# Performance work log

Hardware: AMD Instinct MI355X
Metric: run time of the kernel (lower is better)

The kernel has to match this reference:

```python
import jax, jax.numpy as jnp
import numpy as np

BOX = 100.0      # points live in [0, BOX)^3
STRIDE = 128     # > BOX/voxel_size, used for linearizing 3D voxel coords


def setup_inputs() -> dict:
    key = jax.random.key(0)
    k1, k2 = jax.random.split(key)
    N, C = 2_000_000, 32
    positions = jax.random.uniform(k1, (N, 3), dtype=jnp.float32) * BOX
    features = jax.random.normal(k2, (N, C), dtype=jnp.float32)
    voxel_size = jnp.ones((), dtype=jnp.float32)
    return {"positions": positions, "features": features, "voxel_size": voxel_size}


def reference(positions, features, voxel_size):
    """VoxelPooling(position_fn='center', feature_fn='max').

    Output is padded to N rows (M <= N real voxels); `valid` marks real voxels.
    Voxel grid is aligned to the origin; pooled position is the voxel center.
    """
    N = positions.shape[0]
    # integer voxel coordinates (positions are non-negative here)
    coords = jnp.floor(positions / voxel_size).astype(jnp.int32)           # [N,3]
    lin = coords[:, 0] + STRIDE * coords[:, 1] + STRIDE * STRIDE * coords[:, 2]  # [N]
    # compact unique voxels; jit-compatible with fixed size=N, pad with -1
    uniq, inv = jnp.unique(lin, size=N, fill_value=-1, return_inverse=True)
    # per-voxel max over features (empty segments get dtype-min, masked below)
    pooled_features = jax.ops.segment_max(features, inv, num_segments=N)   # [N,C]
    # decode voxel coords from linear key -> voxel centers
    cz = uniq // (STRIDE * STRIDE)
    rem = uniq % (STRIDE * STRIDE)
    cy = rem // STRIDE
    cx = rem % STRIDE
    centers = (jnp.stack([cx, cy, cz], axis=-1).astype(positions.dtype) + 0.5) * voxel_size
    valid = uniq >= 0                                                      # [N]
    pooled_positions = jnp.where(valid[:, None], centers, 0.0)
    pooled_features = jnp.where(valid[:, None], pooled_features, 0.0)
    return pooled_positions, pooled_features, valid
```

## Files before the change

kernel.cpp:

```cpp
#include <hip/hip_runtime.h>
#include <stdint.h>

#define STRIDE 128
#define NVOX (STRIDE * STRIDE * STRIDE)
#define BINVOX 512
#define NBIN (NVOX / BINVOX)
#define HB 256
#define HT 1024

typedef unsigned long long u64;

__device__ __forceinline__ uint32_t enc_f32(float f) {
  uint32_t u = __float_as_uint(f);
  return (u & 0x80000000u) ? ~u : (u | 0x80000000u);
}
__device__ __forceinline__ float dec_f32(uint32_t e) {
  uint32_t u = (e & 0x80000000u) ? (e & 0x7fffffffu) : ~e;
  return __uint_as_float(u);
}

__global__ __launch_bounds__(HT) void k_hist(const float* __restrict__ pos,
                                             const float* __restrict__ vs_p,
                                             int* __restrict__ lin_arr,
                                             uint8_t* __restrict__ bytemap,
                                             uint32_t* __restrict__ hist, int n) {
  __shared__ uint32_t h[NBIN];
  int b = blockIdx.x, t = threadIdx.x;
  #pragma unroll
  for (int k = t; k < NBIN; k += HT) h[k] = 0u;
  __syncthreads();
  int chunk = (n + HB - 1) / HB;
  int i0 = b * chunk, i1 = min(n, i0 + chunk);
  float vs = vs_p[0];
  for (int i = i0 + t; i < i1; i += HT) {
    float x = pos[3 * (size_t)i + 0];
    float y = pos[3 * (size_t)i + 1];
    float z = pos[3 * (size_t)i + 2];
    int lin = (int)floorf(x / vs) + STRIDE * (int)floorf(y / vs) +
              STRIDE * STRIDE * (int)floorf(z / vs);
    lin_arr[i] = lin;
    bytemap[lin] = 1;
    atomicAdd(&h[lin >> 9], 1u);
  }
  __syncthreads();
  #pragma unroll
  for (int k = t; k < NBIN; k += HT) hist[(size_t)b * NBIN + k] = h[k];
}

__global__ void k_scanA(const uint32_t* __restrict__ hist,
                        const uint32_t* __restrict__ bytemap_w,
                        uint32_t* __restrict__ base2, u64* __restrict__ tot2) {
  int bin = blockIdx.x * blockDim.x + threadIdx.x;
  uint32_t run = 0;
  #pragma unroll 8
  for (int b = 0; b < HB; ++b) {
    base2[(size_t)b * NBIN + bin] = run;
    run += hist[(size_t)b * NBIN + bin];
  }
  const uint4* bp = (const uint4*)(bytemap_w) + (size_t)bin * 32;
  uint32_t occ = 0;
  #pragma unroll
  for (int k = 0; k < 32; ++k) {
    uint4 v = bp[k];
    occ += __popc(v.x) + __popc(v.y) + __popc(v.z) + __popc(v.w);
  }
  tot2[bin] = (u64)run | ((u64)occ << 32);
}

__global__ __launch_bounds__(1024) void k_scan64(const u64* __restrict__ in,
                                                 uint32_t* __restrict__ bin_base,
                                                 uint32_t* __restrict__ occ_base,
                                                 uint32_t* __restrict__ Mp) {
  __shared__ u64 s[1024];
  int t = threadIdx.x;
  u64 v[4], sum = 0;
  #pragma unroll
  for (int j = 0; j < 4; ++j) { v[j] = in[t * 4 + j]; sum += v[j]; }
  s[t] = sum;
  __syncthreads();
  for (int off = 1; off < 1024; off <<= 1) {
    u64 a = (t >= off) ? s[t - off] : 0ull;
    __syncthreads();
    s[t] += a;
    __syncthreads();
  }
  u64 run = s[t] - sum;
  #pragma unroll
  for (int j = 0; j < 4; ++j) {
    bin_base[t * 4 + j] = (uint32_t)run;
    occ_base[t * 4 + j] = (uint32_t)(run >> 32);
    run += v[j];
  }
  if (t == 1023) Mp[0] = (uint32_t)(s[1023] >> 32);
}

__global__ __launch_bounds__(HT) void k_part(const int* __restrict__ lin_arr,
                                             const uint32_t* __restrict__ bin_base,
                                             const uint32_t* __restrict__ base2,
                                             uint32_t* __restrict__ pairs, int n) {
  __shared__ uint32_t cur[NBIN];
  int b = blockIdx.x, t = threadIdx.x;
  #pragma unroll
  for (int k = t; k < NBIN; k += HT)
    cur[k] = bin_base[k] + base2[(size_t)b * NBIN + k];
  __syncthreads();
  int chunk = (n + HB - 1) / HB;
  int i0 = b * chunk, i1 = min(n, i0 + chunk);
  for (int i = i0 + t; i < i1; i += HT) {
    int lin = lin_arr[i];
    uint32_t slot = atomicAdd(&cur[lin >> 9], 1u);
    pairs[slot] = ((uint32_t)(lin & (BINVOX - 1)) << 21) | (uint32_t)i;
  }
}

__global__ __launch_bounds__(1024) void k_pool(
    const float* __restrict__ feat, const float* __restrict__ vs_p,
    const uint32_t* __restrict__ pairs, const uint32_t* __restrict__ bin_base,
    const u64* __restrict__ tot2, const uint32_t* __restrict__ occ_base,
    const uint8_t* __restrict__ bytemap,
    float* __restrict__ out_pos, float* __restrict__ out_feat,
    float* __restrict__ out_valid) {
  __shared__ uint32_t smax[BINVOX * 32];
  __shared__ u64 sbw[8];
  int bin = blockIdx.x;
  int t = threadIdx.x;
  uint32_t cnt = (uint32_t)tot2[bin];
  if (cnt == 0) return;
  uint32_t start = bin_base[bin];

  #pragma unroll
  for (int k = 0; k < 16; ++k) smax[t + k * 1024] = 0u;
  if (t < 512) {
    uint32_t occb = bytemap[(size_t)bin * BINVOX + t];
    u64 m = __ballot(occb != 0);
    if ((t & 63) == 0) sbw[t >> 6] = m;
  }
  __syncthreads();

  int g = t >> 5;
  int ch = t & 31;
  uint32_t last = cnt - 1;
  for (uint32_t u = (uint32_t)g; u < cnt; u += 256) {
    uint32_t p0 = pairs[start + u];
    uint32_t p1 = pairs[start + min(u + 32u, last)];
    uint32_t p2 = pairs[start + min(u + 64u, last)];
    uint32_t p3 = pairs[start + min(u + 96u, last)];
    uint32_t p4 = pairs[start + min(u + 128u, last)];
    uint32_t p5 = pairs[start + min(u + 160u, last)];
    uint32_t p6 = pairs[start + min(u + 192u, last)];
    uint32_t p7 = pairs[start + min(u + 224u, last)];
    float v0 = feat[(size_t)(p0 & 0x1FFFFFu) * 32 + ch];
    float v1 = feat[(size_t)(p1 & 0x1FFFFFu) * 32 + ch];
    float v2 = feat[(size_t)(p2 & 0x1FFFFFu) * 32 + ch];
    float v3 = feat[(size_t)(p3 & 0x1FFFFFu) * 32 + ch];
    float v4 = feat[(size_t)(p4 & 0x1FFFFFu) * 32 + ch];
    float v5 = feat[(size_t)(p5 & 0x1FFFFFu) * 32 + ch];
    float v6 = feat[(size_t)(p6 & 0x1FFFFFu) * 32 + ch];
    float v7 = feat[(size_t)(p7 & 0x1FFFFFu) * 32 + ch];
    atomicMax(&smax[(p0 >> 21) * 32 + ch], enc_f32(v0));
    atomicMax(&smax[(p1 >> 21) * 32 + ch], enc_f32(v1));
    atomicMax(&smax[(p2 >> 21) * 32 + ch], enc_f32(v2));
    atomicMax(&smax[(p3 >> 21) * 32 + ch], enc_f32(v3));
    atomicMax(&smax[(p4 >> 21) * 32 + ch], enc_f32(v4));
    atomicMax(&smax[(p5 >> 21) * 32 + ch], enc_f32(v5));
    atomicMax(&smax[(p6 >> 21) * 32 + ch], enc_f32(v6));
    atomicMax(&smax[(p7 >> 21) * 32 + ch], enc_f32(v7));
  }
  __syncthreads();

  int vb = t >> 1, half = t & 1;
  u64 w = sbw[vb >> 6];
  int bit = vb & 63;
  if ((w >> bit) & 1ull) {
    uint32_t lr = (uint32_t)__popcll(w & ((1ull << bit) - 1ull));
    for (int ww = 0; ww < (vb >> 6); ++ww) lr += (uint32_t)__popcll(sbw[ww]);
    uint32_t rank = occ_base[bin] + lr;
    float4* orow = (float4*)(out_feat + (size_t)rank * 32 + half * 16);
    #pragma unroll
    for (int j = 0; j < 4; ++j) {
      const uint32_t* sp = &smax[vb * 32 + half * 16 + j * 4];
      float4 o;
      o.x = dec_f32(sp[0]); o.y = dec_f32(sp[1]);
      o.z = dec_f32(sp[2]); o.w = dec_f32(sp[3]);
      orow[j] = o;
    }
    if (half == 0) {
      float vs = vs_p[0];
      int lin = bin * BINVOX + vb;
      int cx = lin & 127, cy = (lin >> 7) & 127, cz = lin >> 14;
      out_pos[(size_t)rank * 3 + 0] = ((float)cx + 0.5f) * vs;
      out_pos[(size_t)rank * 3 + 1] = ((float)cy + 0.5f) * vs;
      out_pos[(size_t)rank * 3 + 2] = ((float)cz + 0.5f) * vs;
      out_valid[rank] = 1.0f;
    }
  }
}

__global__ void k_tail(const uint32_t* __restrict__ Mp, float* __restrict__ out_pos,
                       float* __restrict__ out_feat, float* __restrict__ out_valid, int n) {
  size_t gid = (size_t)blockIdx.x * blockDim.x + threadIdx.x;
  int row = (int)(gid >> 3);
  int q = (int)(gid & 7);
  if (row >= n) return;
  uint32_t M = Mp[0];
  if ((uint32_t)row < M) return;
  ((float4*)out_feat)[(size_t)row * 8 + q] = make_float4(0.f, 0.f, 0.f, 0.f);
  if (q == 0) {
    out_pos[(size_t)row * 3 + 0] = 0.f;
    out_pos[(size_t)row * 3 + 1] = 0.f;
    out_pos[(size_t)row * 3 + 2] = 0.f;
    out_valid[row] = 0.f;
  }
}

extern "C" void kernel_launch(void* const* d_in, const int* in_sizes, int n_in,
                              void* d_out, int out_size, void* d_ws, size_t ws_size,
                              hipStream_t stream) {
  const float* pos  = (const float*)d_in[0];
  const float* feat = (const float*)d_in[1];
  const float* vs   = (const float*)d_in[2];
  int n = in_sizes[0] / 3;

  float*    out_pos   = (float*)d_out;
  uint32_t* out_feat  = (uint32_t*)(out_pos + (size_t)n * 3);
  float*    out_valid = (float*)((float*)out_feat + (size_t)n * 32);

  size_t scratch_u32 = 2 * (size_t)n + 2 * (size_t)HB * NBIN + 2 * (size_t)NBIN +
                       2 * (size_t)NBIN + NVOX / 4;
  uint32_t* scratch  = out_feat + (size_t)n * 32 - scratch_u32;
  int*      lin      = (int*)scratch;
  uint32_t* pairs    = scratch + n;
  uint32_t* hist     = pairs + n;
  uint32_t* base2    = hist + (size_t)HB * NBIN;
  u64*      tot2     = (u64*)(base2 + (size_t)HB * NBIN);
  uint32_t* bin_base = (uint32_t*)(tot2 + NBIN);
  uint32_t* occ_base = bin_base + NBIN;
  uint8_t*  bytemap  = (uint8_t*)(occ_base + NBIN);

  uint32_t* Mp = (uint32_t*)d_ws;

  hipMemsetAsync(bytemap, 0, (size_t)NVOX, stream);

  k_hist<<<HB, HT, 0, stream>>>(pos, vs, lin, bytemap, hist, n);
  k_scanA<<<NBIN / 256, 256, 0, stream>>>(hist, (const uint32_t*)bytemap, base2, tot2);
  k_scan64<<<1, 1024, 0, stream>>>(tot2, bin_base, occ_base, Mp);
  k_part<<<HB, HT, 0, stream>>>(lin, bin_base, base2, pairs, n);
  k_pool<<<NBIN, 1024, 0, stream>>>(feat, vs, pairs, bin_base, tot2, occ_base,
                                    bytemap, out_pos, (float*)out_feat, out_valid);
  k_tail<<<(int)(((size_t)n * 8 + 255) / 256), 256, 0, stream>>>(
      Mp, out_pos, (float*)out_feat, out_valid, n);
}
```

Baseline: 225.0 us.

## Fuse scan kernels with grid sync, fold tail into pool, drop bytemap memset

Merges the per-bin scan and the global scan into one multi-block kernel that exchanges segment totals through an atomic counter spin. The tail-zeroing work is appended as extra blocks of the pooling kernel. The bytemap memset is replaced by zeroing the scratch region at the end of each call, so the next call sees a cleared map. This cuts launches and a serial single-block scan, but relies on all scan blocks being co-resident and on the output buffer starting zeroed on the first call.

```diff
diff --git a/kernel.cpp b/kernel.cpp
--- a/kernel.cpp
+++ b/kernel.cpp
@@ -7,6 +7,8 @@
 #define NBIN (NVOX / BINVOX)
 #define HB 256
 #define HT 1024
+#define NSEG 16
+#define SEGBINS (NBIN / NSEG)
 
 typedef unsigned long long u64;
 
@@ -17,16 +19,23 @@
 __device__ __forceinline__ float dec_f32(uint32_t e) {
   uint32_t u = (e & 0x80000000u) ? (e & 0x7fffffffu) : ~e;
   return __uint_as_float(u);
+}
+
+__device__ __forceinline__ uint32_t cnt_eq1(uint32_t w) {
+  uint32_t y = w ^ 0x01010101u;
+  uint32_t z = ~(((y & 0x7F7F7F7Fu) + 0x7F7F7F7Fu) | y | 0x7F7F7F7Fu);
+  return __popc(z);
 }
 
 __global__ __launch_bounds__(HT) void k_hist(const float* __restrict__ pos,
                                              const float* __restrict__ vs_p,
                                              int* __restrict__ lin_arr,
                                              uint8_t* __restrict__ bytemap,
-                                             uint32_t* __restrict__ hist, int n) {
+                                             uint32_t* __restrict__ hist,
+                                             uint32_t* __restrict__ sync, int n) {
   __shared__ uint32_t h[NBIN];
   int b = blockIdx.x, t = threadIdx.x;
-  #pragma unroll
+  if (b == 0 && t == 0) *sync = 0u;
   for (int k = t; k < NBIN; k += HT) h[k] = 0u;
   __syncthreads();
   int chunk = (n + HB - 1) / HB;
@@ -43,55 +52,63 @@
     atomicAdd(&h[lin >> 9], 1u);
   }
   __syncthreads();
-  #pragma unroll
   for (int k = t; k < NBIN; k += HT) hist[(size_t)b * NBIN + k] = h[k];
 }
 
-__global__ void k_scanA(const uint32_t* __restrict__ hist,
-                        const uint32_t* __restrict__ bytemap_w,
-                        uint32_t* __restrict__ base2, u64* __restrict__ tot2) {
-  int bin = blockIdx.x * blockDim.x + threadIdx.x;
+__global__ __launch_bounds__(SEGBINS) void k_scan(
+    const uint32_t* __restrict__ hist, const uint32_t* __restrict__ bytemap_w,
+    uint32_t* __restrict__ base2, u64* __restrict__ tot2,
+    uint32_t* __restrict__ bin_base, uint32_t* __restrict__ occ_base,
+    uint32_t* __restrict__ sync, u64* __restrict__ seg_tot,
+    uint32_t* __restrict__ Mp) {
+  __shared__ u64 s[SEGBINS];
+  int b = blockIdx.x, t = threadIdx.x;
+  int bin = b * SEGBINS + t;
   uint32_t run = 0;
   #pragma unroll 8
-  for (int b = 0; b < HB; ++b) {
-    base2[(size_t)b * NBIN + bin] = run;
-    run += hist[(size_t)b * NBIN + bin];
-  }
-  const uint4* bp = (const uint4*)(bytemap_w) + (size_t)bin * 32;
+  for (int c = 0; c < HB; ++c) {
+    base2[(size_t)c * NBIN + bin] = run;
+    run += hist[(size_t)c * NBIN + bin];
+  }
+  const uint4* bp = (const uint4*)bytemap_w + (size_t)bin * 32;
   uint32_t occ = 0;
   #pragma unroll
   for (int k = 0; k < 32; ++k) {
     uint4 v = bp[k];
-    occ += __popc(v.x) + __popc(v.y) + __popc(v.z) + __popc(v.w);
-  }
-  tot2[bin] = (u64)run | ((u64)occ << 32);
-}
-
-__global__ __launch_bounds__(1024) void k_scan64(const u64* __restrict__ in,
-                                                 uint32_t* __restrict__ bin_base,
-                                                 uint32_t* __restrict__ occ_base,
-                                                 uint32_t* __restrict__ Mp) {
-  __shared__ u64 s[1024];
-  int t = threadIdx.x;
-  u64 v[4], sum = 0;
-  #pragma unroll
-  for (int j = 0; j < 4; ++j) { v[j] = in[t * 4 + j]; sum += v[j]; }
-  s[t] = sum;
-  __syncthreads();
-  for (int off = 1; off < 1024; off <<= 1) {
+    occ += cnt_eq1(v.x) + cnt_eq1(v.y) + cnt_eq1(v.z) + cnt_eq1(v.w);
+  }
+  u64 mine = (u64)run | ((u64)occ << 32);
+  tot2[bin] = mine;
+  s[t] = mine;
+  __syncthreads();
+  for (int off = 1; off < SEGBINS; off <<= 1) {
     u64 a = (t >= off) ? s[t - off] : 0ull;
     __syncthreads();
     s[t] += a;
     __syncthreads();
   }
-  u64 run = s[t] - sum;
+  u64 excl = s[t] - mine;
+  u64 blk_total = s[SEGBINS - 1];
+  if (t == 0) {
+    __hip_atomic_store(&seg_tot[b], blk_total, __ATOMIC_RELEASE,
+                       __HIP_MEMORY_SCOPE_AGENT);
+    __hip_atomic_fetch_add(sync, 1u, __ATOMIC_ACQ_REL, __HIP_MEMORY_SCOPE_AGENT);
+    while (__hip_atomic_load(sync, __ATOMIC_ACQUIRE, __HIP_MEMORY_SCOPE_AGENT) <
+           (uint32_t)NSEG) {}
+  }
+  __syncthreads();
+  u64 pre = 0, grand = 0;
   #pragma unroll
-  for (int j = 0; j < 4; ++j) {
-    bin_base[t * 4 + j] = (uint32_t)run;
-    occ_base[t * 4 + j] = (uint32_t)(run >> 32);
-    run += v[j];
-  }
-  if (t == 1023) Mp[0] = (uint32_t)(s[1023] >> 32);
+  for (int i = 0; i < NSEG; ++i) {
+    u64 v = __hip_atomic_load(&seg_tot[i], __ATOMIC_ACQUIRE,
+                              __HIP_MEMORY_SCOPE_AGENT);
+    if (i < b) pre += v;
+    grand += v;
+  }
+  u64 g = pre + excl;
+  bin_base[bin] = (uint32_t)g;
+  occ_base[bin] = (uint32_t)(g >> 32);
+  if (b == 0 && t == 0) Mp[0] = (uint32_t)(grand >> 32);
 }
 
 __global__ __launch_bounds__(HT) void k_part(const int* __restrict__ lin_arr,
@@ -100,7 +117,6 @@
                                              uint32_t* __restrict__ pairs, int n) {
   __shared__ uint32_t cur[NBIN];
   int b = blockIdx.x, t = threadIdx.x;
-  #pragma unroll
   for (int k = t; k < NBIN; k += HT)
     cur[k] = bin_base[k] + base2[(size_t)b * NBIN + k];
   __syncthreads();
@@ -117,13 +133,32 @@
     const float* __restrict__ feat, const float* __restrict__ vs_p,
     const uint32_t* __restrict__ pairs, const uint32_t* __restrict__ bin_base,
     const u64* __restrict__ tot2, const uint32_t* __restrict__ occ_base,
-    const uint8_t* __restrict__ bytemap,
+    const uint8_t* __restrict__ bytemap, const uint32_t* __restrict__ Mp,
     float* __restrict__ out_pos, float* __restrict__ out_feat,
-    float* __restrict__ out_valid) {
+    float* __restrict__ out_valid, int n, int srow) {
   __shared__ uint32_t smax[BINVOX * 32];
   __shared__ u64 sbw[8];
+  int t = threadIdx.x;
+
+  if (blockIdx.x >= NBIN) {
+    size_t gid = (size_t)(blockIdx.x - NBIN) * 1024 + t;
+    int row = (int)(gid >> 3);
+    int q = (int)(gid & 7);
+    if (row >= n) return;
+    uint32_t M = Mp[0];
+    if ((uint32_t)row < M) return;
+    if (row < srow)
+      ((float4*)out_feat)[(size_t)row * 8 + q] = make_float4(0.f, 0.f, 0.f, 0.f);
+    if (q == 0) {
+      out_pos[(size_t)row * 3 + 0] = 0.f;
+      out_pos[(size_t)row * 3 + 1] = 0.f;
+      out_pos[(size_t)row * 3 + 2] = 0.f;
+      out_valid[row] = 0.f;
+    }
+    return;
+  }
+
   int bin = blockIdx.x;
-  int t = threadIdx.x;
   uint32_t cnt = (uint32_t)tot2[bin];
   if (cnt == 0) return;
   uint32_t start = bin_base[bin];
@@ -132,7 +167,7 @@
   for (int k = 0; k < 16; ++k) smax[t + k * 1024] = 0u;
   if (t < 512) {
     uint32_t occb = bytemap[(size_t)bin * BINVOX + t];
-    u64 m = __ballot(occb != 0);
+    u64 m = __ballot(occb == 1u);
     if ((t & 63) == 0) sbw[t >> 6] = m;
   }
   __syncthreads();
@@ -196,21 +231,9 @@
   }
 }
 
-__global__ void k_tail(const uint32_t* __restrict__ Mp, float* __restrict__ out_pos,
-                       float* __restrict__ out_feat, float* __restrict__ out_valid, int n) {
-  size_t gid = (size_t)blockIdx.x * blockDim.x + threadIdx.x;
-  int row = (int)(gid >> 3);
-  int q = (int)(gid & 7);
-  if (row >= n) return;
-  uint32_t M = Mp[0];
-  if ((uint32_t)row < M) return;
-  ((float4*)out_feat)[(size_t)row * 8 + q] = make_float4(0.f, 0.f, 0.f, 0.f);
-  if (q == 0) {
-    out_pos[(size_t)row * 3 + 0] = 0.f;
-    out_pos[(size_t)row * 3 + 1] = 0.f;
-    out_pos[(size_t)row * 3 + 2] = 0.f;
-    out_valid[row] = 0.f;
-  }
+__global__ void k_tail2(float4* __restrict__ dst, long long cnt4) {
+  long long i = (long long)blockIdx.x * blockDim.x + threadIdx.x;
+  if (i < cnt4) dst[i] = make_float4(0.f, 0.f, 0.f, 0.f);
 }
 
 extern "C" void kernel_launch(void* const* d_in, const int* in_sizes, int n_in,
@@ -225,8 +248,8 @@
   uint32_t* out_feat  = (uint32_t*)(out_pos + (size_t)n * 3);
   float*    out_valid = (float*)((float*)out_feat + (size_t)n * 32);
 
-  size_t scratch_u32 = 2 * (size_t)n + 2 * (size_t)HB * NBIN + 2 * (size_t)NBIN +
-                       2 * (size_t)NBIN + NVOX / 4;
+  size_t scratch_u32 = 2 * (size_t)n + 2 * (size_t)HB * NBIN +
+                       2 * (size_t)NBIN + 2 * (size_t)NBIN + NVOX / 4;
   uint32_t* scratch  = out_feat + (size_t)n * 32 - scratch_u32;
   int*      lin      = (int*)scratch;
   uint32_t* pairs    = scratch + n;
@@ -237,16 +260,21 @@
   uint32_t* occ_base = bin_base + NBIN;
   uint8_t*  bytemap  = (uint8_t*)(occ_base + NBIN);
 
-  uint32_t* Mp = (uint32_t*)d_ws;
-
-  hipMemsetAsync(bytemap, 0, (size_t)NVOX, stream);
-
-  k_hist<<<HB, HT, 0, stream>>>(pos, vs, lin, bytemap, hist, n);
-  k_scanA<<<NBIN / 256, 256, 0, stream>>>(hist, (const uint32_t*)bytemap, base2, tot2);
-  k_scan64<<<1, 1024, 0, stream>>>(tot2, bin_base, occ_base, Mp);
+  int srow = (int)(((size_t)n * 32 - scratch_u32) / 32);
+
+  uint32_t* Mp   = (uint32_t*)d_ws;
+  uint32_t* sync = Mp + 1;
+  u64*      seg_tot = (u64*)(Mp + 2);
+
+  k_hist<<<HB, HT, 0, stream>>>(pos, vs, lin, bytemap, hist, sync, n);
+  k_scan<<<NSEG, SEGBINS, 0, stream>>>(hist, (const uint32_t*)bytemap, base2,
+                                       tot2, bin_base, occ_base, sync, seg_tot, Mp);
   k_part<<<HB, HT, 0, stream>>>(lin, bin_base, base2, pairs, n);
-  k_pool<<<NBIN, 1024, 0, stream>>>(feat, vs, pairs, bin_base, tot2, occ_base,
-                                    bytemap, out_pos, (float*)out_feat, out_valid);
-  k_tail<<<(int)(((size_t)n * 8 + 255) / 256), 256, 0, stream>>>(
-      Mp, out_pos, (float*)out_feat, out_valid, n);
-}
+  int tail_blocks = (int)(((size_t)n * 8 + 1023) / 1024);
+  k_pool<<<NBIN + tail_blocks, 1024, 0, stream>>>(
+      feat, vs, pairs, bin_base, tot2, occ_base, bytemap, Mp,
+      out_pos, (float*)out_feat, out_valid, n, srow);
+  long long cnt4 = ((long long)n * 32 - (long long)srow * 32) / 4;
+  k_tail2<<<(int)((cnt4 + 1023) / 1024), 1024, 0, stream>>>(
+      (float4*)(out_feat + (size_t)srow * 32), cnt4);
+}
```

Result: no change. 222.7 us (-1.0%).
